# Optimization experiments

Measured on AMD Instinct MI355X. Metric: run time of the kernel, lower is better.

The kernel has to match this reference:

```python
import jax, jax.numpy as jnp
import numpy as np

EPS = 1e-12  # F.normalize default eps


def _l2_normalize(x, axis):
    n = jnp.sqrt(jnp.sum(x * x, axis=axis, keepdims=True))
    return x / jnp.maximum(n, EPS)


def setup_inputs() -> dict:
    key = jax.random.key(0)
    k1, k2 = jax.random.split(key)
    code = jax.random.normal(k1, (8, 768, 32, 32), dtype=jnp.float32)
    clusters = jax.random.normal(k2, (64, 768), dtype=jnp.float32)
    return {"code": code, "clusters": clusters, "image_hw": 512}


def reference(code, clusters, image_hw):
    # L2-normalize cluster centroids over channel dim and features over C
    normed_clusters = _l2_normalize(clusters, axis=1)            # [N, C]
    normed_features = _l2_normalize(code, axis=1)                # [B, C, H, W]
    # cosine similarity to every cluster
    inner_products = jnp.einsum('bchw,nc->bnhw', normed_features, normed_clusters)  # [B,N,H,W]
    # hard nearest-cluster assignment -> one-hot over N (channel axis 1)
    assign = jnp.argmax(inner_products, axis=1)                  # [B, H, W] int
    n_classes = clusters.shape[0]
    cluster_probs = jnp.moveaxis(
        jax.nn.one_hot(assign, n_classes, dtype=jnp.float32), -1, 1)  # [B,N,H,W]
    # training loss: negative mean of selected (max) similarity
    cluster_loss = -jnp.mean(jnp.sum(cluster_probs * inner_products, axis=1))
    # resize_to(cluster_probs, image): bilinear upsample to image resolution
    B, N = cluster_probs.shape[0], cluster_probs.shape[1]
    resized = jax.image.resize(cluster_probs, (B, N, image_hw, image_hw), method='bilinear')
    return (cluster_loss, resized, code)
```

## Files before the change

kernel.cpp:

```cpp
#include <hip/hip_runtime.h>

#define CCH 768
#define NCL 64
#define HWIN 1024
#define RES_ELEMS 134217728LL
#define CODE_ELEMS 6291456LL
#define CQUADS 1572863LL
#define ASSIGN_BLOCKS 256
#define COPY_BLOCKS2 512
#define DENSE_BLOCKS 2048

__global__ __launch_bounds__(256) void k_assign(const float* __restrict__ code,
                                                const float* __restrict__ clusters,
                                                int* __restrict__ assign,
                                                float* __restrict__ loss_part,
                                                float* __restrict__ out)
{
    int tid = threadIdx.x;
    int blk = blockIdx.x;

    if (blk >= ASSIGN_BLOCKS) {
        long long u = (long long)(blk - ASSIGN_BLOCKS) * 256 + tid;
        #pragma unroll
        for (int k = 0; k < 12; ++k) {
            long long q = u + (long long)k * (COPY_BLOCKS2 * 256);
            if (q < CQUADS) {
                const float* src = code + 3 + 4 * q;
                float4 v = make_float4(src[0], src[1], src[2], src[3]);
                *(float4*)(out + RES_ELEMS + 4 + 4 * q) = v;
            }
        }
        if (blk == ASSIGN_BLOCKS && tid == 0) {
            out[RES_ELEMS + 1] = code[0];
            out[RES_ELEMS + 2] = code[1];
            out[RES_ELEMS + 3] = code[2];
            out[RES_ELEMS + CODE_ELEMS] = code[CODE_ELEMS - 1];
        }
        return;
    }

    __shared__ float lds_nc[64 * 64];
    __shared__ float lds_red[8 * 2048];
    __shared__ float lds_sq[8 * 32];
    __shared__ float s_scale[64];

    int lane = tid & 63;
    int w = tid >> 6;

    for (int t = 0; t < 16; ++t) {
        int n = w * 16 + t;
        const float* row = clusters + n * CCH;
        float ss = 0.f;
        #pragma unroll
        for (int j = 0; j < 3; ++j) {
            float4 v = *(const float4*)(row + 4 * (lane + 64 * j));
            ss += v.x * v.x + v.y * v.y + v.z * v.z + v.w * v.w;
        }
        #pragma unroll
        for (int m = 1; m < 64; m <<= 1) ss += __shfl_xor(ss, m);
        if (lane == 0) s_scale[n] = 1.0f / fmaxf(sqrtf(ss), 1e-12f);
    }
    __syncthreads();

    int cg = tid >> 5;
    int ng = (tid >> 3) & 3;
    int pg = tid & 7;
    int b = blk >> 5;
    int pixb = (blk & 31) << 5;
    const float* codeB = code + (size_t)b * CCH * HWIN + pixb + (pg << 2);

    int n2 = tid >> 2;
    int qq = tid & 3;
    float myscale = s_scale[n2];

    float acc[4][16];
    #pragma unroll
    for (int p = 0; p < 4; ++p)
        #pragma unroll
        for (int q = 0; q < 16; ++q) acc[p][q] = 0.f;
    float sq0 = 0.f, sq1 = 0.f, sq2 = 0.f, sq3 = 0.f;

    for (int k = 0; k < 12; ++k) {
        __syncthreads();
        const float* srcrow = clusters + n2 * CCH + k * 64 + qq * 16;
        #pragma unroll
        for (int i = 0; i < 4; ++i) {
            float4 v = *(const float4*)(srcrow + 4 * i);
            lds_nc[(qq * 16 + 4 * i + 0) * 64 + n2] = v.x * myscale;
            lds_nc[(qq * 16 + 4 * i + 1) * 64 + n2] = v.y * myscale;
            lds_nc[(qq * 16 + 4 * i + 2) * 64 + n2] = v.z * myscale;
            lds_nc[(qq * 16 + 4 * i + 3) * 64 + n2] = v.w * myscale;
        }
        __syncthreads();
        #pragma unroll
        for (int m = 0; m < 8; ++m) {
            int ch = k * 64 + cg * 8 + m;
            float4 f = *(const float4*)(codeB + ch * HWIN);
            sq0 += f.x * f.x; sq1 += f.y * f.y; sq2 += f.z * f.z; sq3 += f.w * f.w;
            const float* ncrow = lds_nc + ((cg * 8 + m) << 6) + (ng << 4);
            #pragma unroll
            for (int q = 0; q < 16; ++q) {
                float w2 = ncrow[q];
                acc[0][q] += f.x * w2;
                acc[1][q] += f.y * w2;
                acc[2][q] += f.z * w2;
                acc[3][q] += f.w * w2;
            }
        }
    }

    #pragma unroll
    for (int p = 0; p < 4; ++p) {
        float4* dstp = (float4*)&lds_red[cg * 2048 + (pg * 4 + p) * 64 + ng * 16];
        dstp[0] = make_float4(acc[p][0],  acc[p][1],  acc[p][2],  acc[p][3]);
        dstp[1] = make_float4(acc[p][4],  acc[p][5],  acc[p][6],  acc[p][7]);
        dstp[2] = make_float4(acc[p][8],  acc[p][9],  acc[p][10], acc[p][11]);
        dstp[3] = make_float4(acc[p][12], acc[p][13], acc[p][14], acc[p][15]);
    }
    if (ng == 0) {
        lds_sq[cg * 32 + pg * 4 + 0] = sq0;
        lds_sq[cg * 32 + pg * 4 + 1] = sq1;
        lds_sq[cg * 32 + pg * 4 + 2] = sq2;
        lds_sq[cg * 32 + pg * 4 + 3] = sq3;
    }
    __syncthreads();

    for (int idx = tid; idx < 2048; idx += 256) {
        float s = 0.f;
        #pragma unroll
        for (int c2 = 0; c2 < 8; ++c2) s += lds_red[c2 * 2048 + idx];
        lds_nc[idx] = s;
    }
    __syncthreads();

    if (tid < 32) {
        float ss = 0.f;
        #pragma unroll
        for (int c2 = 0; c2 < 8; ++c2) ss += lds_sq[c2 * 32 + tid];
        float inv = 1.0f / fmaxf(sqrtf(ss), 1e-12f);
        float best = -1e30f; int bi = 0;
        for (int n = 0; n < 64; ++n) {
            float v = lds_nc[tid * 64 + n];
            if (v > best) { best = v; bi = n; }
        }
        assign[blk * 32 + tid] = bi;
        float l = best * inv;
        l += __shfl_down(l, 16);
        l += __shfl_down(l, 8);
        l += __shfl_down(l, 4);
        l += __shfl_down(l, 2);
        l += __shfl_down(l, 1);
        if (tid == 0) loss_part[blk] = -l * (1.0f / 8192.0f);
    }
}

__global__ __launch_bounds__(256) void k_dense(const int* __restrict__ assign,
                                               const float* __restrict__ loss_part,
                                               float* __restrict__ out)
{
    int tid = threadIdx.x;
    int blk = blockIdx.x;

    if (blk == 0) {
        __shared__ float lr[4];
        float v = loss_part[tid];
        #pragma unroll
        for (int m = 1; m < 64; m <<= 1) v += __shfl_xor(v, m);
        if ((tid & 63) == 0) lr[tid >> 6] = v;
        __syncthreads();
        if (tid == 0) out[0] = lr[0] + lr[1] + lr[2] + lr[3];
    }

    int b =  blk >> 8;
    int n = (blk >> 2) & 63;
    int c =  blk & 3;
    int I0 = c << 7;
    int rbase = (I0 >> 4) - 1;

    __shared__ unsigned s_mask[10];
    __shared__ int4   s_jj[128];
    __shared__ float4 s_fj[128];

    int lane = tid & 63;
    int w = tid >> 6;

    {
        int r = (w << 1) + (lane >> 5);
        int ir = rbase + r; ir = ir < 0 ? 0 : (ir > 31 ? 31 : ir);
        bool pred = assign[(b << 10) + (ir << 5) + (lane & 31)] == n;
        unsigned long long m = __ballot(pred);
        if (lane == 0) { s_mask[(w << 1)] = (unsigned)m; s_mask[(w << 1) + 1] = (unsigned)(m >> 32); }
    }
    if (w == 0) {
        int r = 8 + (lane >> 5);
        int ir = rbase + r; ir = ir < 0 ? 0 : (ir > 31 ? 31 : ir);
        bool pred = assign[(b << 10) + (ir << 5) + (lane & 31)] == n;
        unsigned long long m = __ballot(pred);
        if (lane == 0) { s_mask[8] = (unsigned)m; s_mask[9] = (unsigned)(m >> 32); }
    }

    if (tid < 128) {
        int s = tid;
        int jl[4];
        if (s == 0) { jl[0] = 0; jl[1] = 1; jl[2] = 2; jl[3] = 511; }
        else { jl[0] = 4 * s - 1; jl[1] = 4 * s; jl[2] = 4 * s + 1; jl[3] = 4 * s + 2; }
        int pj[4]; float fjv[4];
        #pragma unroll
        for (int k = 0; k < 4; ++k) {
            int j = jl[k];
            float xj = (j + 0.5f) * 0.0625f - 0.5f;
            float fjf = floorf(xj);
            int jj = (int)fjf;
            fjv[k] = xj - fjf;
            int j0 = jj < 0 ? 0 : jj;
            int j1 = (jj + 1) > 31 ? 31 : (jj + 1);
            pj[k] = j0 | (j1 << 8);
        }
        s_jj[s] = make_int4(pj[0], pj[1], pj[2], pj[3]);
        s_fj[s] = make_float4(fjv[0], fjv[1], fjv[2], fjv[3]);
    }
    __syncthreads();

    int rr = tid >> 7;
    int s  = tid & 127;
    int4   pj4 = s_jj[s];
    float4 fj4 = s_fj[s];
    int   j0a[4] = { pj4.x & 255, pj4.y & 255, pj4.z & 255, pj4.w & 255 };
    int   j1a[4] = { pj4.x >> 8,  pj4.y >> 8,  pj4.z >> 8,  pj4.w >> 8 };
    float fja[4] = { fj4.x, fj4.y, fj4.z, fj4.w };

    long long planebase = 1LL + ((long long)b << 24) + ((long long)n << 18);

    for (int r2 = 0; r2 < 64; ++r2) {
        int i = I0 + (r2 << 1) + rr;
        float xi = (i + 0.5f) * 0.0625f - 0.5f;
        float fif = floorf(xi);
        int ii = (int)fif;
        float fi = xi - fif;
        float fi1 = 1.0f - fi;
        unsigned m0 = s_mask[ii - rbase];
        unsigned m1 = s_mask[ii - rbase + 1];
        float v[4];
        #pragma unroll
        for (int k = 0; k < 4; ++k) {
            float b00 = (float)((m0 >> j0a[k]) & 1u);
            float b01 = (float)((m0 >> j1a[k]) & 1u);
            float b10 = (float)((m1 >> j0a[k]) & 1u);
            float b11 = (float)((m1 >> j1a[k]) & 1u);
            float P = fi1 * b00 + fi * b10;
            float Q = fi1 * b01 + fi * b11;
            v[k] = P + fja[k] * (Q - P);
        }
        float* rowbase = out + planebase + ((long long)i << 9);
        if (s == 0) {
            rowbase[0] = v[0]; rowbase[1] = v[1]; rowbase[2] = v[2]; rowbase[511] = v[3];
        } else {
            *(float4*)(rowbase + 4 * s - 1) = make_float4(v[0], v[1], v[2], v[3]);
        }
    }
}

extern "C" void kernel_launch(void* const* d_in, const int* in_sizes, int n_in,
                              void* d_out, int out_size, void* d_ws, size_t ws_size,
                              hipStream_t stream)
{
    const float* code     = (const float*)d_in[0];
    const float* clusters = (const float*)d_in[1];
    float* out = (float*)d_out;
    int* assign = (int*)d_ws;
    float* loss_part = (float*)((char*)d_ws + 32768);

    k_assign<<<ASSIGN_BLOCKS + COPY_BLOCKS2, 256, 0, stream>>>(code, clusters, assign, loss_part, out);
    k_dense <<<DENSE_BLOCKS,                 256, 0, stream>>>(assign, loss_part, out);
}
```

Before: 618.7 us.

## Replace LDS cross-group reduction with wave shuffles and swizzle cluster tile

Remaps the thread roles so the eight channel groups sit inside one wavefront, which lets the partial dot products and squared norms be reduced with shuffle-xor instead of a 64KB LDS staging buffer. The cluster tile in LDS is XOR-swizzled and read as float4 to cut bank conflicts and the number of LDS loads. Launch bounds now request 4 blocks per CU, which occupancy the smaller LDS footprint makes possible. The trade-off is many extra shuffle instructions (64 accumulators times 3 steps) and register pressure from the occupancy hint, and this only touches the assignment kernel, while the large dense upsample write probably dominates runtime.

```diff
diff --git a/kernel.cpp b/kernel.cpp
--- a/kernel.cpp
+++ b/kernel.cpp
@@ -10,11 +10,11 @@
 #define COPY_BLOCKS2 512
 #define DENSE_BLOCKS 2048
 
-__global__ __launch_bounds__(256) void k_assign(const float* __restrict__ code,
-                                                const float* __restrict__ clusters,
-                                                int* __restrict__ assign,
-                                                float* __restrict__ loss_part,
-                                                float* __restrict__ out)
+__global__ __launch_bounds__(256, 4) void k_assign(const float* __restrict__ code,
+                                                   const float* __restrict__ clusters,
+                                                   int* __restrict__ assign,
+                                                   float* __restrict__ loss_part,
+                                                   float* __restrict__ out)
 {
     int tid = threadIdx.x;
     int blk = blockIdx.x;
@@ -40,8 +40,7 @@
     }
 
     __shared__ float lds_nc[64 * 64];
-    __shared__ float lds_red[8 * 2048];
-    __shared__ float lds_sq[8 * 32];
+    __shared__ float lds_sq[32];
     __shared__ float s_scale[64];
 
     int lane = tid & 63;
@@ -62,9 +61,9 @@
     }
     __syncthreads();
 
-    int cg = tid >> 5;
-    int ng = (tid >> 3) & 3;
     int pg = tid & 7;
+    int cg = (tid >> 3) & 7;
+    int ng = tid >> 6;
     int b = blk >> 5;
     int pixb = (blk & 31) << 5;
     const float* codeB = code + (size_t)b * CCH * HWIN + pixb + (pg << 2);
@@ -86,57 +85,71 @@
         #pragma unroll
         for (int i = 0; i < 4; ++i) {
             float4 v = *(const float4*)(srcrow + 4 * i);
-            lds_nc[(qq * 16 + 4 * i + 0) * 64 + n2] = v.x * myscale;
-            lds_nc[(qq * 16 + 4 * i + 1) * 64 + n2] = v.y * myscale;
-            lds_nc[(qq * 16 + 4 * i + 2) * 64 + n2] = v.z * myscale;
-            lds_nc[(qq * 16 + 4 * i + 3) * 64 + n2] = v.w * myscale;
+            int c0 = qq * 16 + 4 * i;
+            lds_nc[(c0 + 0) * 64 + (n2 ^ (((c0 + 0) >> 3) << 2))] = v.x * myscale;
+            lds_nc[(c0 + 1) * 64 + (n2 ^ (((c0 + 1) >> 3) << 2))] = v.y * myscale;
+            lds_nc[(c0 + 2) * 64 + (n2 ^ (((c0 + 2) >> 3) << 2))] = v.z * myscale;
+            lds_nc[(c0 + 3) * 64 + (n2 ^ (((c0 + 3) >> 3) << 2))] = v.w * myscale;
         }
         __syncthreads();
         #pragma unroll
         for (int m = 0; m < 8; ++m) {
-            int ch = k * 64 + cg * 8 + m;
-            float4 f = *(const float4*)(codeB + ch * HWIN);
+            int chl = cg * 8 + m;
+            float4 f = *(const float4*)(codeB + (size_t)(k * 64 + chl) * HWIN);
             sq0 += f.x * f.x; sq1 += f.y * f.y; sq2 += f.z * f.z; sq3 += f.w * f.w;
-            const float* ncrow = lds_nc + ((cg * 8 + m) << 6) + (ng << 4);
+            const float* basep = lds_nc + (chl << 6);
             #pragma unroll
-            for (int q = 0; q < 16; ++q) {
-                float w2 = ncrow[q];
-                acc[0][q] += f.x * w2;
-                acc[1][q] += f.y * w2;
-                acc[2][q] += f.z * w2;
-                acc[3][q] += f.w * w2;
+            for (int u = 0; u < 4; ++u) {
+                float4 wv = *(const float4*)(basep + (((ng * 16 + 4 * u) ^ (cg << 2))));
+                float wl[4] = { wv.x, wv.y, wv.z, wv.w };
+                #pragma unroll
+                for (int v2 = 0; v2 < 4; ++v2) {
+                    float w2 = wl[v2];
+                    int q = 4 * u + v2;
+                    acc[0][q] += f.x * w2;
+                    acc[1][q] += f.y * w2;
+                    acc[2][q] += f.z * w2;
+                    acc[3][q] += f.w * w2;
+                }
             }
         }
     }
 
     #pragma unroll
-    for (int p = 0; p < 4; ++p) {
-        float4* dstp = (float4*)&lds_red[cg * 2048 + (pg * 4 + p) * 64 + ng * 16];
-        dstp[0] = make_float4(acc[p][0],  acc[p][1],  acc[p][2],  acc[p][3]);
-        dstp[1] = make_float4(acc[p][4],  acc[p][5],  acc[p][6],  acc[p][7]);
-        dstp[2] = make_float4(acc[p][8],  acc[p][9],  acc[p][10], acc[p][11]);
-        dstp[3] = make_float4(acc[p][12], acc[p][13], acc[p][14], acc[p][15]);
-    }
-    if (ng == 0) {
-        lds_sq[cg * 32 + pg * 4 + 0] = sq0;
-        lds_sq[cg * 32 + pg * 4 + 1] = sq1;
-        lds_sq[cg * 32 + pg * 4 + 2] = sq2;
-        lds_sq[cg * 32 + pg * 4 + 3] = sq3;
-    }
-    __syncthreads();
-
-    for (int idx = tid; idx < 2048; idx += 256) {
-        float s = 0.f;
-        #pragma unroll
-        for (int c2 = 0; c2 < 8; ++c2) s += lds_red[c2 * 2048 + idx];
-        lds_nc[idx] = s;
+    for (int mask = 8; mask <= 32; mask <<= 1) {
+        #pragma unroll
+        for (int p = 0; p < 4; ++p)
+            #pragma unroll
+            for (int q = 0; q < 16; ++q)
+                acc[p][q] += __shfl_xor(acc[p][q], mask);
+        sq0 += __shfl_xor(sq0, mask);
+        sq1 += __shfl_xor(sq1, mask);
+        sq2 += __shfl_xor(sq2, mask);
+        sq3 += __shfl_xor(sq3, mask);
+    }
+
+    __syncthreads();
+
+    if (cg == 0) {
+        #pragma unroll
+        for (int p = 0; p < 4; ++p) {
+            float* d = &lds_nc[(pg * 4 + p) * 64 + ng * 16];
+            *(float4*)(d + 0)  = make_float4(acc[p][0],  acc[p][1],  acc[p][2],  acc[p][3]);
+            *(float4*)(d + 4)  = make_float4(acc[p][4],  acc[p][5],  acc[p][6],  acc[p][7]);
+            *(float4*)(d + 8)  = make_float4(acc[p][8],  acc[p][9],  acc[p][10], acc[p][11]);
+            *(float4*)(d + 12) = make_float4(acc[p][12], acc[p][13], acc[p][14], acc[p][15]);
+        }
+        if (ng == 0) {
+            lds_sq[pg * 4 + 0] = sq0;
+            lds_sq[pg * 4 + 1] = sq1;
+            lds_sq[pg * 4 + 2] = sq2;
+            lds_sq[pg * 4 + 3] = sq3;
+        }
     }
     __syncthreads();
 
     if (tid < 32) {
-        float ss = 0.f;
-        #pragma unroll
-        for (int c2 = 0; c2 < 8; ++c2) ss += lds_sq[c2 * 32 + tid];
+        float ss = lds_sq[tid];
         float inv = 1.0f / fmaxf(sqrtf(ss), 1e-12f);
         float best = -1e30f; int bi = 0;
         for (int n = 0; n < 64; ++n) {
```

Result: slower. 662.8 us (+7.1%).
